# Optimization experiments

Hardware: AMD Instinct MI355X
Metric: run time of the kernel (lower is better)

## Reference

```python
import jax, jax.numpy as jnp
import numpy as np

IMG_H, IMG_W = 800.0, 1280.0
STRIDE = 16
SCALE = 1.0 / STRIDE
P, S = 14, 1              # pooler resolution, sampling ratio
NUM_CLASSES = 80
BBOX_W = (10.0, 10.0, 5.0, 5.0)
SCORE_TH, NMS_TH, MAX_DET, IOU_TH = 0.05, 0.5, 100, 0.5
SCALE_CLAMP = float(np.log(1000.0 / 16.0))


def _make_boxes(key, n_img, n_box):
    k1, k2, k3, k4 = jax.random.split(key, 4)
    x1 = jax.random.uniform(k1, (n_img, n_box)) * (IMG_W - 64.0)
    y1 = jax.random.uniform(k2, (n_img, n_box)) * (IMG_H - 64.0)
    w = jax.random.uniform(k3, (n_img, n_box)) * 300.0 + 16.0
    h = jax.random.uniform(k4, (n_img, n_box)) * 300.0 + 16.0
    x2 = jnp.minimum(x1 + w, IMG_W)
    y2 = jnp.minimum(y1 + h, IMG_H)
    return jnp.stack([x1, y1, x2, y2], axis=-1)


def setup_inputs() -> dict:
    key = jax.random.key(0)
    ks = jax.random.split(key, 6)
    features = jax.random.normal(ks[0], (2, 50, 80, 1024), dtype=jnp.float32)
    proposals = _make_boxes(ks[1], 2, 256)
    gt_boxes = _make_boxes(ks[2], 2, 64)
    gt_classes = jax.random.randint(ks[3], (2, 64), 0, NUM_CLASSES)
    W_cls = jax.random.normal(ks[4], (1024, NUM_CLASSES + 1), dtype=jnp.float32) * 0.01
    b_cls = jnp.zeros((NUM_CLASSES + 1,), jnp.float32)
    W_box = jax.random.normal(ks[5], (1024, 4), dtype=jnp.float32) * 0.01
    b_box = jnp.zeros((4,), jnp.float32)
    return {"features": features, "proposals": proposals, "gt_boxes": gt_boxes,
            "gt_classes": gt_classes, "W_cls": W_cls, "b_cls": b_cls,
            "W_box": W_box, "b_box": b_box}


def pairwise_iou(a, b):
    # a: [G,4], b: [R,4], boxes as (x1,y1,x2,y2) -> [G,R]
    area_a = (a[:, 2] - a[:, 0]) * (a[:, 3] - a[:, 1])
    area_b = (b[:, 2] - b[:, 0]) * (b[:, 3] - b[:, 1])
    lt = jnp.maximum(a[:, None, :2], b[None, :, :2])
    rb = jnp.minimum(a[:, None, 2:], b[None, :, 2:])
    wh = jnp.clip(rb - lt, 0.0)
    inter = wh[..., 0] * wh[..., 1]
    return inter / jnp.maximum(area_a[:, None] + area_b[None, :] - inter, 1e-9)


def roi_align_one(feat, boxes):
    # feat: [H,W,C], boxes: [R,4] in image coords -> pooled [R,P,P,C]
    H, W, C = feat.shape
    b = boxes * SCALE
    x1, y1, x2, y2 = b[:, 0], b[:, 1], b[:, 2], b[:, 3]
    off = (jnp.arange(S, dtype=feat.dtype) + 0.5) / S       # [S]
    grid = jnp.arange(P, dtype=feat.dtype)                   # [P]
    bh = ((y2 - y1) / P)[:, None, None]
    bw = ((x2 - x1) / P)[:, None, None]
    # aligned RoIAlign sample coords (half-pixel offset)
    gy = y1[:, None, None] + (grid[None, :, None] + off[None, None, :]) * bh - 0.5  # [R,P,S]
    gx = x1[:, None, None] + (grid[None, :, None] + off[None, None, :]) * bw - 0.5
    gy = jnp.clip(gy, 0.0, H - 1.0)
    gx = jnp.clip(gx, 0.0, W - 1.0)
    y0 = jnp.floor(gy); x0 = jnp.floor(gx)
    y0i = y0.astype(jnp.int32); x0i = x0.astype(jnp.int32)
    y1i = jnp.minimum(y0i + 1, H - 1); x1i = jnp.minimum(x0i + 1, W - 1)
    ly = gy - y0; lx = gx - x0

    def g(yi, xi):  # cross-product gather -> [R,P,S,P,S,C]
        return feat[yi[:, :, :, None, None], xi[:, None, None, :, :]]

    wy0 = (1.0 - ly)[:, :, :, None, None, None]; wy1 = ly[:, :, :, None, None, None]
    wx0 = (1.0 - lx)[:, None, None, :, :, None]; wx1 = lx[:, None, None, :, :, None]
    val = wy0 * (wx0 * g(y0i, x0i) + wx1 * g(y0i, x1i)) \
        + wy1 * (wx0 * g(y1i, x0i) + wx1 * g(y1i, x1i))
    return val.mean(axis=(2, 4))  # average sampling points per bin -> [R,P,P,C]


def decode_boxes(deltas, boxes):
    wx, wy, ww, wh = BBOX_W
    widths = boxes[..., 2] - boxes[..., 0]
    heights = boxes[..., 3] - boxes[..., 1]
    ctr_x = boxes[..., 0] + 0.5 * widths
    ctr_y = boxes[..., 1] + 0.5 * heights
    dx = deltas[..., 0] / wx
    dy = deltas[..., 1] / wy
    dw = jnp.minimum(deltas[..., 2] / ww, SCALE_CLAMP)
    dh = jnp.minimum(deltas[..., 3] / wh, SCALE_CLAMP)
    pcx = dx * widths + ctr_x
    pcy = dy * heights + ctr_y
    pw = jnp.exp(dw) * widths
    ph = jnp.exp(dh) * heights
    out = jnp.stack([pcx - 0.5 * pw, pcy - 0.5 * ph, pcx + 0.5 * pw, pcy + 0.5 * ph], axis=-1)
    lim = jnp.array([IMG_W, IMG_H, IMG_W, IMG_H], out.dtype)
    return jnp.clip(out, 0.0, lim)


def nms_keep(boxes, scores):
    # greedy class-agnostic NMS, fixed-size keep mask [R]
    R = scores.shape[0]
    order = jnp.argsort(-scores)
    sb = boxes[order]
    iou = pairwise_iou(sb, sb)
    idx = jnp.arange(R)

    def body(i, keep):
        suppressed = jnp.any((idx < i) & keep & (iou[:, i] > NMS_TH))
        return keep.at[i].set(jnp.logical_not(suppressed))

    keep_sorted = jax.lax.fori_loop(0, R, body, jnp.ones((R,), bool))
    return jnp.zeros((R,), bool).at[order].set(keep_sorted)


def reference(features, proposals, gt_boxes, gt_classes, W_cls, b_cls, W_box, b_box):
    N, R = proposals.shape[:2]
    # --- proposal <-> gt matching (training-side labeling) ---
    iou_m = jax.vmap(pairwise_iou)(gt_boxes, proposals)          # [N,G,R]
    matched_vals = iou_m.max(axis=1)
    matched_idxs = iou_m.argmax(axis=1)                          # [N,R]
    match_labels = (matched_vals >= IOU_TH).astype(jnp.int32)    # [N,R] fg=1/bg=0
    # --- RoIAlign pooling on the single C4 feature map ---
    pooled = jax.vmap(roi_align_one)(features, proposals)        # [N,R,P,P,C]
    feat_vec = pooled.mean(axis=(2, 3))                          # res5 surrogate global avg -> [N,R,C]
    # --- box predictor ---
    scores_all = jax.nn.softmax(feat_vec @ W_cls + b_cls, axis=-1)
    fg_scores = scores_all[..., :NUM_CLASSES].max(axis=-1)       # drop background column
    deltas = feat_vec @ W_box + b_box
    boxes = decode_boxes(deltas, proposals)                      # [N,R,4]
    # --- score threshold + NMS + top-k ---
    keep = jax.vmap(nms_keep)(boxes, fg_scores) & (fg_scores > SCORE_TH)
    masked = jnp.where(keep, fg_scores, -jnp.inf)
    rank = jnp.argsort(jnp.argsort(-masked, axis=-1), axis=-1)
    keep = keep & (rank < MAX_DET)
    det = jnp.concatenate([boxes, fg_scores[..., None], keep.astype(boxes.dtype)[..., None]], axis=-1)
    return det, matched_idxs, match_labels
```

## Files before the change

kernel.cpp:

```cpp
#include <hip/hip_runtime.h>
#include <math.h>

#define N_IMG 2
#define R_PROP 256
#define G_GT 64
#define C_CH 1024
#define FH 50
#define FW 80
#define P_POOL 14
#define NCLS 80
#define IMG_W_F 1280.0f
#define IMG_H_F 800.0f
#define SCALE_F 0.0625f
#define SCORE_TH_F 0.05f
#define NMS_TH_F 0.5f
#define IOU_TH_F 0.5f
#define MAX_DET_I 100
#define SCALE_CLAMP_F 4.135166556742356f

__global__ __launch_bounds__(512) void prep_kernel(
    const float* __restrict__ proposals,
    const float* __restrict__ gt_boxes,
    int* __restrict__ perm,
    float* __restrict__ out_idx,
    float* __restrict__ out_lbl) {
  const int t = threadIdx.x;
  const int n = t >> 8;
  __shared__ float cy[N_IMG * R_PROP];
  const float* pb = proposals + (size_t)t * 4;
  float bx1 = pb[0], by1 = pb[1], bx2 = pb[2], by2 = pb[3];
  cy[t] = by1 + by2;
  __syncthreads();

  {
    float my = cy[t];
    int rk = 0;
    const int base = n * R_PROP;
#pragma unroll 8
    for (int j = base; j < base + R_PROP; ++j) {
      float cj = cy[j];
      rk += (cj < my) || (cj == my && j < t);
    }
    perm[base + rk] = t & 255;
  }

  {
    float area_b = (bx2 - bx1) * (by2 - by1);
    float best = -1.0f;
    int bidx = 0;
    const float* gt = gt_boxes + (size_t)n * G_GT * 4;
#pragma unroll 4
    for (int g = 0; g < G_GT; ++g) {
      float gx1 = gt[g * 4 + 0], gy1 = gt[g * 4 + 1];
      float gx2 = gt[g * 4 + 2], gy2 = gt[g * 4 + 3];
      float area_a = (gx2 - gx1) * (gy2 - gy1);
      float ix1 = fmaxf(gx1, bx1), iy1 = fmaxf(gy1, by1);
      float ix2 = fminf(gx2, bx2), iy2 = fminf(gy2, by2);
      float iw = fmaxf(ix2 - ix1, 0.0f), ih = fmaxf(iy2 - iy1, 0.0f);
      float inter = iw * ih;
      float iou = inter / fmaxf(area_a + area_b - inter, 1e-9f);
      if (iou > best) { best = iou; bidx = g; }
    }
    out_idx[t] = (float)bidx;
    out_lbl[t] = (best >= IOU_TH_F) ? 1.0f : 0.0f;
  }
}

__global__ __launch_bounds__(1024) void roihead_kernel(
    const float* __restrict__ features,
    const float* __restrict__ proposals,
    const int* __restrict__ perm,
    const float* __restrict__ W_cls,
    const float* __restrict__ b_cls,
    const float* __restrict__ W_box,
    const float* __restrict__ b_box,
    float* __restrict__ boxes_dec,
    float* __restrict__ scores) {
  const int b = blockIdx.x;
  const int xcd = b & 7;
  const int slot = b >> 3;
  const int n = xcd >> 2;
  const int band = xcd & 3;
  const int blk = n * R_PROP + perm[n * R_PROP + band * 64 + slot];

  const float* feat = features + (size_t)n * (FH * FW * C_CH);
  const int t = threadIdx.x;
  const int c4 = t & 255;
  const int g = t >> 8;

  __shared__ float s_Wy[FH];
  __shared__ float s_Wx[FW];
  __shared__ int s_b[4];
  __shared__ float4 s_red[3][256];
  __shared__ __align__(16) float sf[C_CH];
  __shared__ float s_part[12][85];
  __shared__ float sl[85];
  __shared__ float s_r2[8];

  if (t < FH) s_Wy[t] = 0.0f;
  if (t >= 128 && t < 128 + FW) s_Wx[t - 128] = 0.0f;
  __syncthreads();

  if (t < 2 * P_POOL) {
    const float* pb = proposals + (size_t)blk * 4;
    bool isY = t < P_POOL;
    int i = isY ? t : t - P_POOL;
    float lo = isY ? pb[1] : pb[0];
    float hi = isY ? pb[3] : pb[2];
    float limit = isY ? (float)(FH - 1) : (float)(FW - 1);
    float b1 = lo * SCALE_F, b2 = hi * SCALE_F;
    float bs = (b2 - b1) * (1.0f / P_POOL);
    float gg = b1 + ((float)i + 0.5f) * bs - 0.5f;
    gg = fminf(fmaxf(gg, 0.0f), limit);
    float fl = floorf(gg);
    int i0 = (int)fl;
    int i1 = min(i0 + 1, (int)limit);
    float l = gg - fl;
    if (isY) {
      atomicAdd(&s_Wy[i0], 1.0f - l);
      atomicAdd(&s_Wy[i1], l);
      if (i == 0) s_b[0] = i0;
      if (i == P_POOL - 1) s_b[1] = i1;
    } else {
      atomicAdd(&s_Wx[i0], 1.0f - l);
      atomicAdd(&s_Wx[i1], l);
      if (i == 0) s_b[2] = i0;
      if (i == P_POOL - 1) s_b[3] = i1;
    }
  }
  __syncthreads();

  {
    const int ylo = s_b[0], yhi = s_b[1], xlo = s_b[2], xhi = s_b[3];
    float4 acc = make_float4(0.f, 0.f, 0.f, 0.f);
    for (int y = ylo + g; y <= yhi; y += 4) {
      float wy = s_Wy[y];
      const float4* row = (const float4*)(feat + (size_t)y * (FW * C_CH)) + c4;
#pragma unroll 8
      for (int x = xlo; x <= xhi; ++x) {
        float w = wy * s_Wx[x];
        float4 f = row[x * (C_CH / 4)];
        acc.x += w * f.x;
        acc.y += w * f.y;
        acc.z += w * f.z;
        acc.w += w * f.w;
      }
    }
    if (g > 0) s_red[g - 1][c4] = acc;
    __syncthreads();
    if (g == 0) {
      float4 a0 = s_red[0][c4];
      float4 a1 = s_red[1][c4];
      float4 a2 = s_red[2][c4];
      const float inv = 1.0f / (float)(P_POOL * P_POOL);
      float4 r;
      r.x = (acc.x + a0.x + a1.x + a2.x) * inv;
      r.y = (acc.y + a0.y + a1.y + a2.y) * inv;
      r.z = (acc.z + a0.z + a1.z + a2.z) * inv;
      r.w = (acc.w + a0.w + a1.w + a2.w) * inv;
      ((float4*)sf)[c4] = r;
    }
    __syncthreads();
  }

  const int kq = t / 85;
  const int j = t - kq * 85;
  if (kq < 12) {
    float acc = 0.0f;
    if (j < 81) {
      const float* __restrict__ w = W_cls + j;
#pragma unroll 8
      for (int k = kq; k < C_CH; k += 12) acc += sf[k] * w[k * 81];
    } else {
      const float* __restrict__ w = W_box + (j - 81);
#pragma unroll 8
      for (int k = kq; k < C_CH; k += 12) acc += sf[k] * w[k * 4];
    }
    s_part[kq][j] = acc;
  }
  __syncthreads();

  if (t < 85) {
    float acc = (t < 81) ? b_cls[t] : b_box[t - 81];
#pragma unroll
    for (int p = 0; p < 12; ++p) acc += s_part[p][t];
    sl[t] = acc;
  }
  __syncthreads();

  if (t < 128) {
    float xm = (t < 81) ? sl[t] : -INFINITY;
    float xf = (t < NCLS) ? sl[t] : -INFINITY;
#pragma unroll
    for (int off = 32; off; off >>= 1) {
      xm = fmaxf(xm, __shfl_down(xm, off, 64));
      xf = fmaxf(xf, __shfl_down(xf, off, 64));
    }
    if ((t & 63) == 0) { s_r2[t >> 6] = xm; s_r2[2 + (t >> 6)] = xf; }
  }
  __syncthreads();
  const float m = fmaxf(s_r2[0], s_r2[1]);
  if (t < 128) {
    float xs = (t < 81) ? expf(sl[t] - m) : 0.0f;
#pragma unroll
    for (int off = 32; off; off >>= 1) xs += __shfl_down(xs, off, 64);
    if ((t & 63) == 0) s_r2[4 + (t >> 6)] = xs;
  }
  __syncthreads();

  if (t == 0) {
    float sum = s_r2[4] + s_r2[5];
    float fgm = fmaxf(s_r2[2], s_r2[3]);
    scores[blk] = expf(fgm - m) / sum;

    const float* pb = proposals + (size_t)blk * 4;
    float w = pb[2] - pb[0], h = pb[3] - pb[1];
    float cx = pb[0] + 0.5f * w, cy = pb[1] + 0.5f * h;
    float dx = sl[81] * 0.1f;
    float dy = sl[82] * 0.1f;
    float dw = fminf(sl[83] * 0.2f, SCALE_CLAMP_F);
    float dh = fminf(sl[84] * 0.2f, SCALE_CLAMP_F);
    float pcx = dx * w + cx, pcy = dy * h + cy;
    float pw = expf(dw) * w, ph = expf(dh) * h;
    float ox1 = fminf(fmaxf(pcx - 0.5f * pw, 0.0f), IMG_W_F);
    float oy1 = fminf(fmaxf(pcy - 0.5f * ph, 0.0f), IMG_H_F);
    float ox2 = fminf(fmaxf(pcx + 0.5f * pw, 0.0f), IMG_W_F);
    float oy2 = fminf(fmaxf(pcy + 0.5f * ph, 0.0f), IMG_H_F);
    float* bd = boxes_dec + (size_t)blk * 4;
    bd[0] = ox1; bd[1] = oy1; bd[2] = ox2; bd[3] = oy2;
  }
}

__global__ __launch_bounds__(1024) void nms_kernel(
    const float* __restrict__ boxes_dec,
    const float* __restrict__ scores,
    float* __restrict__ det) {
  const int n = blockIdx.x;
  const int u = threadIdx.x;
  const int i = u & 255;
  const int q = u >> 8;
  const int j40 = q * 16;

  __shared__ __align__(16) float ss[R_PROP];
  __shared__ float4 sbs[R_PROP];
  __shared__ int s_part[4 * R_PROP];
  __shared__ int s_rank[R_PROP];
  __shared__ __align__(16) unsigned long long s_mask[R_PROP * 4];
  __shared__ unsigned long long s_keep[4];
  __shared__ __align__(16) float sm[R_PROP];

  float4 myb;
  float mys;
  if (q == 0) {
    myb = ((const float4*)boxes_dec)[n * R_PROP + i];
    mys = scores[n * R_PROP + i];
    ss[i] = mys;
  }
  __syncthreads();

  {
    float s = ss[i];
    int cnt = 0;
#pragma unroll
    for (int j4 = j40; j4 < j40 + 16; ++j4) {
      float4 v = ((const float4*)ss)[j4];
      int jb = j4 * 4;
      cnt += (v.x > s) || (v.x == s && jb + 0 < i);
      cnt += (v.y > s) || (v.y == s && jb + 1 < i);
      cnt += (v.z > s) || (v.z == s && jb + 2 < i);
      cnt += (v.w > s) || (v.w == s && jb + 3 < i);
    }
    s_part[q * R_PROP + i] = cnt;
  }
  __syncthreads();
  if (q == 0) {
    int rk = s_part[i] + s_part[R_PROP + i] + s_part[2 * R_PROP + i] +
             s_part[3 * R_PROP + i];
    s_rank[i] = rk;
    sbs[rk] = myb;
  }
  __syncthreads();

  {
    float4 bi = sbs[i];
    float area_i = (bi.z - bi.x) * (bi.w - bi.y);
    unsigned long long m = 0;
    const int j0 = q * 64;
#pragma unroll 8
    for (int jj = 0; jj < 64; ++jj) {
      float4 bj = sbs[j0 + jj];
      float area_j = (bj.z - bj.x) * (bj.w - bj.y);
      float ix1 = fmaxf(bi.x, bj.x), iy1 = fmaxf(bi.y, bj.y);
      float ix2 = fminf(bi.z, bj.z), iy2 = fminf(bi.w, bj.w);
      float iw = fmaxf(ix2 - ix1, 0.0f), ih = fmaxf(iy2 - iy1, 0.0f);
      float inter = iw * ih;
      float iou = inter / fmaxf(area_i + area_j - inter, 1e-9f);
      m |= (iou > NMS_TH_F) ? (1ull << jj) : 0ull;
    }
    s_mask[i * 4 + q] = m;
  }
  __syncthreads();

  if (u == 0) {
    unsigned long long K0 = ~0ull, K1 = ~0ull, K2 = ~0ull, K3 = ~0ull;
#pragma unroll 16
    for (int b = 1; b < 64; ++b) {
      unsigned long long m0 = s_mask[(size_t)b * 4 + 0];
      unsigned long long sup = m0 & K0 & ((1ull << b) - 1ull);
      K0 = sup ? (K0 & ~(1ull << b)) : K0;
    }
#pragma unroll 16
    for (int b = 0; b < 64; ++b) {
      const unsigned long long* mi = &s_mask[(size_t)(64 + b) * 4];
      unsigned long long m0 = mi[0], m1 = mi[1];
      unsigned long long sup = (m0 & K0) | (m1 & K1 & ((1ull << b) - 1ull));
      K1 = sup ? (K1 & ~(1ull << b)) : K1;
    }
#pragma unroll 16
    for (int b = 0; b < 64; ++b) {
      const unsigned long long* mi = &s_mask[(size_t)(128 + b) * 4];
      unsigned long long m0 = mi[0], m1 = mi[1], m2 = mi[2];
      unsigned long long sup =
          (m0 & K0) | (m1 & K1) | (m2 & K2 & ((1ull << b) - 1ull));
      K2 = sup ? (K2 & ~(1ull << b)) : K2;
    }
#pragma unroll 16
    for (int b = 0; b < 64; ++b) {
      const unsigned long long* mi = &s_mask[(size_t)(192 + b) * 4];
      unsigned long long m0 = mi[0], m1 = mi[1], m2 = mi[2], m3 = mi[3];
      unsigned long long sup = (m0 & K0) | (m1 & K1) | (m2 & K2) |
                               (m3 & K3 & ((1ull << b) - 1ull));
      K3 = sup ? (K3 & ~(1ull << b)) : K3;
    }
    s_keep[0] = K0; s_keep[1] = K1; s_keep[2] = K2; s_keep[3] = K3;
  }
  __syncthreads();

  bool kept = false;
  if (q == 0) {
    int rk = s_rank[i];
    kept = ((s_keep[rk >> 6] >> (rk & 63)) & 1ull) && (mys > SCORE_TH_F);
    sm[i] = kept ? mys : -INFINITY;
  }
  __syncthreads();

  {
    float mym = sm[i];
    int cnt = 0;
#pragma unroll
    for (int j4 = j40; j4 < j40 + 16; ++j4) {
      float4 v = ((const float4*)sm)[j4];
      int jb = j4 * 4;
      cnt += (v.x > mym) || (v.x == mym && jb + 0 < i);
      cnt += (v.y > mym) || (v.y == mym && jb + 1 < i);
      cnt += (v.z > mym) || (v.z == mym && jb + 2 < i);
      cnt += (v.w > mym) || (v.w == mym && jb + 3 < i);
    }
    s_part[q * R_PROP + i] = cnt;
  }
  __syncthreads();

  if (q == 0) {
    int rk2 = s_part[i] + s_part[R_PROP + i] + s_part[2 * R_PROP + i] +
              s_part[3 * R_PROP + i];
    kept = kept && (rk2 < MAX_DET_I);
    float* dr = det + ((size_t)n * R_PROP + i) * 6;
    dr[0] = myb.x; dr[1] = myb.y; dr[2] = myb.z; dr[3] = myb.w;
    dr[4] = mys;
    dr[5] = kept ? 1.0f : 0.0f;
  }
}

extern "C" void kernel_launch(void* const* d_in, const int* in_sizes, int n_in,
                              void* d_out, int out_size, void* d_ws, size_t ws_size,
                              hipStream_t stream) {
  const float* features  = (const float*)d_in[0];
  const float* proposals = (const float*)d_in[1];
  const float* gt_boxes  = (const float*)d_in[2];
  const float* W_cls = (const float*)d_in[4];
  const float* b_cls = (const float*)d_in[5];
  const float* W_box = (const float*)d_in[6];
  const float* b_box = (const float*)d_in[7];

  float* out = (float*)d_out;
  float* out_det = out;
  float* out_idx = out + N_IMG * R_PROP * 6;
  float* out_lbl = out_idx + N_IMG * R_PROP;

  float* boxes_dec = (float*)d_ws;
  float* scores    = boxes_dec + (size_t)N_IMG * R_PROP * 4;
  int*   perm      = (int*)(scores + N_IMG * R_PROP);

  prep_kernel<<<1, 512, 0, stream>>>(proposals, gt_boxes, perm, out_idx, out_lbl);
  roihead_kernel<<<N_IMG * R_PROP, 1024, 0, stream>>>(
      features, proposals, perm, W_cls, b_cls, W_box, b_box, boxes_dec, scores);
  nms_kernel<<<N_IMG, 1024, 0, stream>>>(boxes_dec, scores, out_det);
}
```

Before: 167.8 us.

## Split RoI head channels across two blocks and move softmax/decode into NMS kernel

Each RoI is now handled by two blocks, each pooling and projecting half of the 1024 channels with 8 row-groups of 128 threads. The blocks write partial logits to a workspace buffer instead of finishing the work themselves. The NMS kernel sums the two halves, adds the biases, and computes the softmax, foreground score and box decode per proposal. This doubles parallelism in the gather-bound pooling stage and shortens each block's serial tail. The cost is a larger workspace round trip and more serial work in the two-block NMS kernel.

```diff
diff --git a/kernel.cpp b/kernel.cpp
--- a/kernel.cpp
+++ b/kernel.cpp
@@ -71,31 +71,27 @@
     const float* __restrict__ proposals,
     const int* __restrict__ perm,
     const float* __restrict__ W_cls,
-    const float* __restrict__ b_cls,
     const float* __restrict__ W_box,
-    const float* __restrict__ b_box,
-    float* __restrict__ boxes_dec,
-    float* __restrict__ scores) {
+    float* __restrict__ part) {
   const int b = blockIdx.x;
   const int xcd = b & 7;
   const int slot = b >> 3;
   const int n = xcd >> 2;
   const int band = xcd & 3;
-  const int blk = n * R_PROP + perm[n * R_PROP + band * 64 + slot];
-
-  const float* feat = features + (size_t)n * (FH * FW * C_CH);
+  const int h = slot & 1;
+  const int blk = n * R_PROP + perm[n * R_PROP + band * 64 + (slot >> 1)];
+
+  const float* feat = features + (size_t)n * (FH * FW * C_CH) + h * (C_CH / 2);
   const int t = threadIdx.x;
-  const int c4 = t & 255;
-  const int g = t >> 8;
+  const int c4 = t & 127;
+  const int g = t >> 7;
 
   __shared__ float s_Wy[FH];
   __shared__ float s_Wx[FW];
   __shared__ int s_b[4];
-  __shared__ float4 s_red[3][256];
-  __shared__ __align__(16) float sf[C_CH];
+  __shared__ float4 s_red[7][128];
+  __shared__ __align__(16) float sf[C_CH / 2];
   __shared__ float s_part[12][85];
-  __shared__ float sl[85];
-  __shared__ float s_r2[8];
 
   if (t < FH) s_Wy[t] = 0.0f;
   if (t >= 128 && t < 128 + FW) s_Wx[t - 128] = 0.0f;
@@ -133,7 +129,7 @@
   {
     const int ylo = s_b[0], yhi = s_b[1], xlo = s_b[2], xhi = s_b[3];
     float4 acc = make_float4(0.f, 0.f, 0.f, 0.f);
-    for (int y = ylo + g; y <= yhi; y += 4) {
+    for (int y = ylo + g; y <= yhi; y += 8) {
       float wy = s_Wy[y];
       const float4* row = (const float4*)(feat + (size_t)y * (FW * C_CH)) + c4;
 #pragma unroll 8
@@ -149,16 +145,14 @@
     if (g > 0) s_red[g - 1][c4] = acc;
     __syncthreads();
     if (g == 0) {
-      float4 a0 = s_red[0][c4];
-      float4 a1 = s_red[1][c4];
-      float4 a2 = s_red[2][c4];
       const float inv = 1.0f / (float)(P_POOL * P_POOL);
-      float4 r;
-      r.x = (acc.x + a0.x + a1.x + a2.x) * inv;
-      r.y = (acc.y + a0.y + a1.y + a2.y) * inv;
-      r.z = (acc.z + a0.z + a1.z + a2.z) * inv;
-      r.w = (acc.w + a0.w + a1.w + a2.w) * inv;
-      ((float4*)sf)[c4] = r;
+#pragma unroll
+      for (int p = 0; p < 7; ++p) {
+        float4 a = s_red[p][c4];
+        acc.x += a.x; acc.y += a.y; acc.z += a.z; acc.w += a.w;
+      }
+      ((float4*)sf)[c4] =
+          make_float4(acc.x * inv, acc.y * inv, acc.z * inv, acc.w * inv);
     }
     __syncthreads();
   }
@@ -167,73 +161,33 @@
   const int j = t - kq * 85;
   if (kq < 12) {
     float acc = 0.0f;
+    const int kbase = h * (C_CH / 2);
     if (j < 81) {
-      const float* __restrict__ w = W_cls + j;
+      const float* __restrict__ w = W_cls + (size_t)kbase * 81 + j;
 #pragma unroll 8
-      for (int k = kq; k < C_CH; k += 12) acc += sf[k] * w[k * 81];
+      for (int k = kq; k < C_CH / 2; k += 12) acc += sf[k] * w[k * 81];
     } else {
-      const float* __restrict__ w = W_box + (j - 81);
+      const float* __restrict__ w = W_box + (size_t)kbase * 4 + (j - 81);
 #pragma unroll 8
-      for (int k = kq; k < C_CH; k += 12) acc += sf[k] * w[k * 4];
+      for (int k = kq; k < C_CH / 2; k += 12) acc += sf[k] * w[k * 4];
     }
     s_part[kq][j] = acc;
   }
   __syncthreads();
 
   if (t < 85) {
-    float acc = (t < 81) ? b_cls[t] : b_box[t - 81];
+    float acc = 0.0f;
 #pragma unroll
     for (int p = 0; p < 12; ++p) acc += s_part[p][t];
-    sl[t] = acc;
-  }
-  __syncthreads();
-
-  if (t < 128) {
-    float xm = (t < 81) ? sl[t] : -INFINITY;
-    float xf = (t < NCLS) ? sl[t] : -INFINITY;
-#pragma unroll
-    for (int off = 32; off; off >>= 1) {
-      xm = fmaxf(xm, __shfl_down(xm, off, 64));
-      xf = fmaxf(xf, __shfl_down(xf, off, 64));
-    }
-    if ((t & 63) == 0) { s_r2[t >> 6] = xm; s_r2[2 + (t >> 6)] = xf; }
-  }
-  __syncthreads();
-  const float m = fmaxf(s_r2[0], s_r2[1]);
-  if (t < 128) {
-    float xs = (t < 81) ? expf(sl[t] - m) : 0.0f;
-#pragma unroll
-    for (int off = 32; off; off >>= 1) xs += __shfl_down(xs, off, 64);
-    if ((t & 63) == 0) s_r2[4 + (t >> 6)] = xs;
-  }
-  __syncthreads();
-
-  if (t == 0) {
-    float sum = s_r2[4] + s_r2[5];
-    float fgm = fmaxf(s_r2[2], s_r2[3]);
-    scores[blk] = expf(fgm - m) / sum;
-
-    const float* pb = proposals + (size_t)blk * 4;
-    float w = pb[2] - pb[0], h = pb[3] - pb[1];
-    float cx = pb[0] + 0.5f * w, cy = pb[1] + 0.5f * h;
-    float dx = sl[81] * 0.1f;
-    float dy = sl[82] * 0.1f;
-    float dw = fminf(sl[83] * 0.2f, SCALE_CLAMP_F);
-    float dh = fminf(sl[84] * 0.2f, SCALE_CLAMP_F);
-    float pcx = dx * w + cx, pcy = dy * h + cy;
-    float pw = expf(dw) * w, ph = expf(dh) * h;
-    float ox1 = fminf(fmaxf(pcx - 0.5f * pw, 0.0f), IMG_W_F);
-    float oy1 = fminf(fmaxf(pcy - 0.5f * ph, 0.0f), IMG_H_F);
-    float ox2 = fminf(fmaxf(pcx + 0.5f * pw, 0.0f), IMG_W_F);
-    float oy2 = fminf(fmaxf(pcy + 0.5f * ph, 0.0f), IMG_H_F);
-    float* bd = boxes_dec + (size_t)blk * 4;
-    bd[0] = ox1; bd[1] = oy1; bd[2] = ox2; bd[3] = oy2;
+    part[(size_t)blk * 170 + h * 85 + t] = acc;
   }
 }
 
 __global__ __launch_bounds__(1024) void nms_kernel(
-    const float* __restrict__ boxes_dec,
-    const float* __restrict__ scores,
+    const float* __restrict__ part,
+    const float* __restrict__ proposals,
+    const float* __restrict__ b_cls,
+    const float* __restrict__ b_box,
     float* __restrict__ det) {
   const int n = blockIdx.x;
   const int u = threadIdx.x;
@@ -248,12 +202,68 @@
   __shared__ __align__(16) unsigned long long s_mask[R_PROP * 4];
   __shared__ unsigned long long s_keep[4];
   __shared__ __align__(16) float sm[R_PROP];
+  __shared__ float s_f1[4 * R_PROP];
+  __shared__ float s_f2[4 * R_PROP];
+  __shared__ float s_m[R_PROP];
+
+  const float* pp = part + ((size_t)n * R_PROP + i) * 170;
+
+  {
+    float pm = -INFINITY, pf = -INFINITY;
+    for (int j = q; j < 81; j += 4) {
+      float v = pp[j] + pp[85 + j] + b_cls[j];
+      pm = fmaxf(pm, v);
+      if (j < NCLS) pf = fmaxf(pf, v);
+    }
+    s_f1[q * R_PROP + i] = pm;
+    s_f2[q * R_PROP + i] = pf;
+  }
+  __syncthreads();
+  if (q == 0) {
+    float m = fmaxf(fmaxf(s_f1[i], s_f1[R_PROP + i]),
+                    fmaxf(s_f1[2 * R_PROP + i], s_f1[3 * R_PROP + i]));
+    s_m[i] = m;
+  }
+  __syncthreads();
+
+  {
+    float mm = s_m[i];
+    float ps = 0.0f;
+    for (int j = q; j < 81; j += 4) {
+      float v = pp[j] + pp[85 + j] + b_cls[j];
+      ps += expf(v - mm);
+    }
+    s_f1[q * R_PROP + i] = ps;
+  }
+  __syncthreads();
 
   float4 myb;
   float mys;
   if (q == 0) {
-    myb = ((const float4*)boxes_dec)[n * R_PROP + i];
-    mys = scores[n * R_PROP + i];
+    float mm = s_m[i];
+    float sum = s_f1[i] + s_f1[R_PROP + i] + s_f1[2 * R_PROP + i] +
+                s_f1[3 * R_PROP + i];
+    float fgm = fmaxf(fmaxf(s_f2[i], s_f2[R_PROP + i]),
+                      fmaxf(s_f2[2 * R_PROP + i], s_f2[3 * R_PROP + i]));
+    mys = expf(fgm - mm) / sum;
+
+    const float* pb = proposals + ((size_t)n * R_PROP + i) * 4;
+    float w = pb[2] - pb[0], h = pb[3] - pb[1];
+    float cx = pb[0] + 0.5f * w, cy = pb[1] + 0.5f * h;
+    float d0 = pp[81] + pp[85 + 81] + b_box[0];
+    float d1 = pp[82] + pp[85 + 82] + b_box[1];
+    float d2 = pp[83] + pp[85 + 83] + b_box[2];
+    float d3 = pp[84] + pp[85 + 84] + b_box[3];
+    float dx = d0 * 0.1f;
+    float dy = d1 * 0.1f;
+    float dw = fminf(d2 * 0.2f, SCALE_CLAMP_F);
+    float dh = fminf(d3 * 0.2f, SCALE_CLAMP_F);
+    float pcx = dx * w + cx, pcy = dy * h + cy;
+    float pw = expf(dw) * w, ph = expf(dh) * h;
+    myb.x = fminf(fmaxf(pcx - 0.5f * pw, 0.0f), IMG_W_F);
+    myb.y = fminf(fmaxf(pcy - 0.5f * ph, 0.0f), IMG_H_F);
+    myb.z = fminf(fmaxf(pcx + 0.5f * pw, 0.0f), IMG_W_F);
+    myb.w = fminf(fmaxf(pcy + 0.5f * ph, 0.0f), IMG_H_F);
     ss[i] = mys;
   }
   __syncthreads();
@@ -387,12 +397,11 @@
   float* out_idx = out + N_IMG * R_PROP * 6;
   float* out_lbl = out_idx + N_IMG * R_PROP;
 
-  float* boxes_dec = (float*)d_ws;
-  float* scores    = boxes_dec + (size_t)N_IMG * R_PROP * 4;
-  int*   perm      = (int*)(scores + N_IMG * R_PROP);
+  float* part = (float*)d_ws;
+  int*   perm = (int*)(part + (size_t)N_IMG * R_PROP * 170);
 
   prep_kernel<<<1, 512, 0, stream>>>(proposals, gt_boxes, perm, out_idx, out_lbl);
-  roihead_kernel<<<N_IMG * R_PROP, 1024, 0, stream>>>(
-      features, proposals, perm, W_cls, b_cls, W_box, b_box, boxes_dec, scores);
-  nms_kernel<<<N_IMG, 1024, 0, stream>>>(boxes_dec, scores, out_det);
+  roihead_kernel<<<2 * N_IMG * R_PROP, 1024, 0, stream>>>(
+      features, proposals, perm, W_cls, W_box, part);
+  nms_kernel<<<N_IMG, 1024, 0, stream>>>(part, proposals, b_cls, b_box, out_det);
 }
```

Measured after the change: 206.9 us. 23.3% more time.

## Split RoI pooling across two channel halves per proposal with finalize kernel

Applied to the files above, without the earlier changes.

Each proposal is now handled by two blocks, each pooling and projecting half of the 1024 channels, with 8 row groups instead of 4 per block. Partial logits go to a workspace buffer, and a new finalize kernel sums them, adds the biases, and does the softmax and box decoding. This doubles the block count to improve occupancy and spread the bandwidth-heavy gather across more CUs. In exchange it adds an extra kernel launch, a global round trip for the partials, and more cross-block reduction overhead.

```diff
diff --git a/kernel.cpp b/kernel.cpp
--- a/kernel.cpp
+++ b/kernel.cpp
@@ -71,31 +71,27 @@
     const float* __restrict__ proposals,
     const int* __restrict__ perm,
     const float* __restrict__ W_cls,
-    const float* __restrict__ b_cls,
     const float* __restrict__ W_box,
-    const float* __restrict__ b_box,
-    float* __restrict__ boxes_dec,
-    float* __restrict__ scores) {
+    float* __restrict__ part) {
   const int b = blockIdx.x;
   const int xcd = b & 7;
   const int slot = b >> 3;
   const int n = xcd >> 2;
   const int band = xcd & 3;
-  const int blk = n * R_PROP + perm[n * R_PROP + band * 64 + slot];
-
-  const float* feat = features + (size_t)n * (FH * FW * C_CH);
+  const int h = slot & 1;
+  const int blk = n * R_PROP + perm[n * R_PROP + band * 64 + (slot >> 1)];
+
+  const float* feat = features + (size_t)n * (FH * FW * C_CH) + h * (C_CH / 2);
   const int t = threadIdx.x;
-  const int c4 = t & 255;
-  const int g = t >> 8;
+  const int c4 = t & 127;
+  const int g = t >> 7;
 
   __shared__ float s_Wy[FH];
   __shared__ float s_Wx[FW];
   __shared__ int s_b[4];
-  __shared__ float4 s_red[3][256];
-  __shared__ __align__(16) float sf[C_CH];
+  __shared__ float4 s_red[7][128];
+  __shared__ __align__(16) float sf[C_CH / 2];
   __shared__ float s_part[12][85];
-  __shared__ float sl[85];
-  __shared__ float s_r2[8];
 
   if (t < FH) s_Wy[t] = 0.0f;
   if (t >= 128 && t < 128 + FW) s_Wx[t - 128] = 0.0f;
@@ -133,7 +129,7 @@
   {
     const int ylo = s_b[0], yhi = s_b[1], xlo = s_b[2], xhi = s_b[3];
     float4 acc = make_float4(0.f, 0.f, 0.f, 0.f);
-    for (int y = ylo + g; y <= yhi; y += 4) {
+    for (int y = ylo + g; y <= yhi; y += 8) {
       float wy = s_Wy[y];
       const float4* row = (const float4*)(feat + (size_t)y * (FW * C_CH)) + c4;
 #pragma unroll 8
@@ -149,16 +145,14 @@
     if (g > 0) s_red[g - 1][c4] = acc;
     __syncthreads();
     if (g == 0) {
-      float4 a0 = s_red[0][c4];
-      float4 a1 = s_red[1][c4];
-      float4 a2 = s_red[2][c4];
       const float inv = 1.0f / (float)(P_POOL * P_POOL);
-      float4 r;
-      r.x = (acc.x + a0.x + a1.x + a2.x) * inv;
-      r.y = (acc.y + a0.y + a1.y + a2.y) * inv;
-      r.z = (acc.z + a0.z + a1.z + a2.z) * inv;
-      r.w = (acc.w + a0.w + a1.w + a2.w) * inv;
-      ((float4*)sf)[c4] = r;
+#pragma unroll
+      for (int p = 0; p < 7; ++p) {
+        float4 a = s_red[p][c4];
+        acc.x += a.x; acc.y += a.y; acc.z += a.z; acc.w += a.w;
+      }
+      ((float4*)sf)[c4] =
+          make_float4(acc.x * inv, acc.y * inv, acc.z * inv, acc.w * inv);
     }
     __syncthreads();
   }
@@ -167,28 +161,48 @@
   const int j = t - kq * 85;
   if (kq < 12) {
     float acc = 0.0f;
+    const int kbase = h * (C_CH / 2);
     if (j < 81) {
-      const float* __restrict__ w = W_cls + j;
+      const float* __restrict__ w = W_cls + (size_t)kbase * 81 + j;
 #pragma unroll 8
-      for (int k = kq; k < C_CH; k += 12) acc += sf[k] * w[k * 81];
+      for (int k = kq; k < C_CH / 2; k += 12) acc += sf[k] * w[k * 81];
     } else {
-      const float* __restrict__ w = W_box + (j - 81);
+      const float* __restrict__ w = W_box + (size_t)kbase * 4 + (j - 81);
 #pragma unroll 8
-      for (int k = kq; k < C_CH; k += 12) acc += sf[k] * w[k * 4];
+      for (int k = kq; k < C_CH / 2; k += 12) acc += sf[k] * w[k * 4];
     }
     s_part[kq][j] = acc;
   }
   __syncthreads();
 
   if (t < 85) {
-    float acc = (t < 81) ? b_cls[t] : b_box[t - 81];
+    float acc = 0.0f;
 #pragma unroll
     for (int p = 0; p < 12; ++p) acc += s_part[p][t];
-    sl[t] = acc;
-  }
-  __syncthreads();
-
-  if (t < 128) {
+    part[(size_t)blk * 170 + h * 85 + t] = acc;
+  }
+}
+
+__global__ __launch_bounds__(128) void finalize_kernel(
+    const float* __restrict__ part,
+    const float* __restrict__ proposals,
+    const float* __restrict__ b_cls,
+    const float* __restrict__ b_box,
+    float* __restrict__ boxes_dec,
+    float* __restrict__ scores) {
+  const int blk = blockIdx.x;
+  const int t = threadIdx.x;
+  __shared__ float sl[85];
+  __shared__ float s_red[8];
+
+  const float* pp = part + (size_t)blk * 170;
+  if (t < 85) {
+    float bias = (t < 81) ? b_cls[t] : b_box[t - 81];
+    sl[t] = pp[t] + pp[85 + t] + bias;
+  }
+  __syncthreads();
+
+  {
     float xm = (t < 81) ? sl[t] : -INFINITY;
     float xf = (t < NCLS) ? sl[t] : -INFINITY;
 #pragma unroll
@@ -196,21 +210,21 @@
       xm = fmaxf(xm, __shfl_down(xm, off, 64));
       xf = fmaxf(xf, __shfl_down(xf, off, 64));
     }
-    if ((t & 63) == 0) { s_r2[t >> 6] = xm; s_r2[2 + (t >> 6)] = xf; }
-  }
-  __syncthreads();
-  const float m = fmaxf(s_r2[0], s_r2[1]);
-  if (t < 128) {
+    if ((t & 63) == 0) { s_red[t >> 6] = xm; s_red[2 + (t >> 6)] = xf; }
+  }
+  __syncthreads();
+  const float m = fmaxf(s_red[0], s_red[1]);
+  {
     float xs = (t < 81) ? expf(sl[t] - m) : 0.0f;
 #pragma unroll
     for (int off = 32; off; off >>= 1) xs += __shfl_down(xs, off, 64);
-    if ((t & 63) == 0) s_r2[4 + (t >> 6)] = xs;
+    if ((t & 63) == 0) s_red[4 + (t >> 6)] = xs;
   }
   __syncthreads();
 
   if (t == 0) {
-    float sum = s_r2[4] + s_r2[5];
-    float fgm = fmaxf(s_r2[2], s_r2[3]);
+    float sum = s_red[4] + s_red[5];
+    float fgm = fmaxf(s_red[2], s_red[3]);
     scores[blk] = expf(fgm - m) / sum;
 
     const float* pb = proposals + (size_t)blk * 4;
@@ -387,12 +401,15 @@
   float* out_idx = out + N_IMG * R_PROP * 6;
   float* out_lbl = out_idx + N_IMG * R_PROP;
 
-  float* boxes_dec = (float*)d_ws;
+  float* part      = (float*)d_ws;
+  float* boxes_dec = part + (size_t)N_IMG * R_PROP * 170;
   float* scores    = boxes_dec + (size_t)N_IMG * R_PROP * 4;
   int*   perm      = (int*)(scores + N_IMG * R_PROP);
 
   prep_kernel<<<1, 512, 0, stream>>>(proposals, gt_boxes, perm, out_idx, out_lbl);
-  roihead_kernel<<<N_IMG * R_PROP, 1024, 0, stream>>>(
-      features, proposals, perm, W_cls, b_cls, W_box, b_box, boxes_dec, scores);
+  roihead_kernel<<<2 * N_IMG * R_PROP, 1024, 0, stream>>>(
+      features, proposals, perm, W_cls, W_box, part);
+  finalize_kernel<<<N_IMG * R_PROP, 128, 0, stream>>>(
+      part, proposals, b_cls, b_box, boxes_dec, scores);
   nms_kernel<<<N_IMG, 1024, 0, stream>>>(boxes_dec, scores, out_det);
 }
```

Measured after the change: 166.8 us, median of 2. No clear change (-0.6%).
